# Optimization experiments

Measured on AMD Instinct MI355X. Metric: run time of the kernel, lower is better.

Reference implementation:

```python
import jax, jax.numpy as jnp
import numpy as np

N_NODES = 50000
N_EDGES = 1600000
IN_FEATS = 256
NUM_HEADS = 4
OUT_FEATS = 32
NEG_SLOPE = 0.2


def setup_inputs() -> dict:
    key = jax.random.key(0)
    k_feat, k_src, k_dst, k_w, k_al, k_ar = jax.random.split(key, 6)
    feat = jax.random.normal(k_feat, (N_NODES, IN_FEATS), dtype=jnp.float32)
    src = jax.random.randint(k_src, (N_EDGES,), 0, N_NODES, dtype=jnp.int32)
    dst = jax.random.randint(k_dst, (N_EDGES,), 0, N_NODES, dtype=jnp.int32)
    # Glorot/xavier-like scales
    w_scale = np.sqrt(2.0 / (IN_FEATS + NUM_HEADS * OUT_FEATS)).astype(np.float32)
    a_scale = np.sqrt(2.0 / (1 + OUT_FEATS)).astype(np.float32)
    W_fc = jax.random.normal(k_w, (NUM_HEADS * OUT_FEATS, IN_FEATS), dtype=jnp.float32) * w_scale
    attn_l = jax.random.normal(k_al, (1, NUM_HEADS, OUT_FEATS), dtype=jnp.float32) * a_scale
    attn_r = jax.random.normal(k_ar, (1, NUM_HEADS, OUT_FEATS), dtype=jnp.float32) * a_scale
    bias = jnp.zeros((NUM_HEADS * OUT_FEATS,), dtype=jnp.float32)
    return {"feat": feat, "W_fc": W_fc, "attn_l": attn_l, "attn_r": attn_r,
            "bias": bias, "src": src, "dst": dst}


def reference(feat, W_fc, attn_l, attn_r, bias, src, dst):
    N = feat.shape[0]
    H, F = NUM_HEADS, OUT_FEATS
    # dense projection: [N, H, F]
    h = (feat @ W_fc.T).reshape(N, H, F)
    # per-node attention logits: [N, H]
    el = (h * attn_l).sum(axis=-1)
    er = (h * attn_r).sum(axis=-1)
    # u_add_v edge score + leaky relu: [E, H]
    e = el[src] + er[dst]
    e = jnp.where(e >= 0, e, NEG_SLOPE * e)
    # segment softmax over destination nodes
    m = jax.ops.segment_max(e, dst, num_segments=N)          # [N, H]
    m = jnp.where(jnp.isfinite(m), m, 0.0)                   # guard 0-in-degree
    e_exp = jnp.exp(e - m[dst])                              # [E, H]
    denom = jax.ops.segment_sum(e_exp, dst, num_segments=N)  # [N, H]
    denom = jnp.where(denom > 0, denom, 1.0)
    a = e_exp / denom[dst]                                   # [E, H]
    # weighted message aggregation: [N, H, F]
    msg = h[src] * a[:, :, None]                             # [E, H, F]
    out = jax.ops.segment_sum(msg, dst, num_segments=N)
    out = out + bias.reshape(1, H, F)
    return out
```

## Files before the change

kernel.cpp:

```cpp
#include <hip/hip_runtime.h>

typedef __attribute__((ext_vector_type(8))) short bf16x8;
typedef __attribute__((ext_vector_type(4))) float f32x4;

#define IN_F 256
#define HF 128
#define NHEADS 4
#define NEG 0.2f
#define GBM 128
#define GBK 64
#define LDK 72

#define RB 256
#define NBP 200
#define CHUNK 6400
#define ITPT 25
#define BCAP 10000

__device__ __forceinline__ unsigned short f2bf(float x) {
    unsigned u = __float_as_uint(x);
    unsigned r = (u + 0x7FFFu + ((u >> 16) & 1u)) >> 16;
    return (unsigned short)r;
}
__device__ __forceinline__ float bf2f(unsigned short b) {
    return __uint_as_float((unsigned)b << 16);
}

__global__ __launch_bounds__(256) void gemm_kernel(const float* __restrict__ feat,
                                                   const float* __restrict__ W,
                                                   unsigned short* __restrict__ hb, int N) {
    __shared__ unsigned short As[GBM][LDK];
    __shared__ unsigned short Bs[HF][LDK];
    const int t = threadIdx.x;
    const int n0 = blockIdx.x * GBM;
    const int lane = t & 63;
    const int wid = t >> 6;
    const int wm = (wid >> 1) * 64;
    const int wn = (wid & 1) * 64;
    const int lr = lane & 15;
    const int lk = (lane >> 4) * 8;

    f32x4 acc[4][4];
#pragma unroll
    for (int i = 0; i < 4; i++)
#pragma unroll
        for (int j = 0; j < 4; j++) acc[i][j] = (f32x4){0.f, 0.f, 0.f, 0.f};

    for (int k0 = 0; k0 < IN_F; k0 += GBK) {
#pragma unroll
        for (int r = 0; r < 4; r++) {
            int idx = t + r * 256;
            int row = idx >> 3;
            int c8 = (idx & 7) * 8;
            int n = n0 + row;
            float4 v0 = make_float4(0.f, 0.f, 0.f, 0.f), v1 = v0;
            if (n < N) {
                v0 = *(const float4*)&feat[(size_t)n * IN_F + k0 + c8];
                v1 = *(const float4*)&feat[(size_t)n * IN_F + k0 + c8 + 4];
            }
            bf16x8 sa;
            sa[0] = f2bf(v0.x); sa[1] = f2bf(v0.y); sa[2] = f2bf(v0.z); sa[3] = f2bf(v0.w);
            sa[4] = f2bf(v1.x); sa[5] = f2bf(v1.y); sa[6] = f2bf(v1.z); sa[7] = f2bf(v1.w);
            *(bf16x8*)&As[row][c8] = sa;
            float4 w0 = *(const float4*)&W[(size_t)row * IN_F + k0 + c8];
            float4 w1 = *(const float4*)&W[(size_t)row * IN_F + k0 + c8 + 4];
            bf16x8 sb;
            sb[0] = f2bf(w0.x); sb[1] = f2bf(w0.y); sb[2] = f2bf(w0.z); sb[3] = f2bf(w0.w);
            sb[4] = f2bf(w1.x); sb[5] = f2bf(w1.y); sb[6] = f2bf(w1.z); sb[7] = f2bf(w1.w);
            *(bf16x8*)&Bs[row][c8] = sb;
        }
        __syncthreads();
#pragma unroll
        for (int ks = 0; ks < 2; ks++) {
            bf16x8 a[4], b[4];
#pragma unroll
            for (int mi = 0; mi < 4; mi++) a[mi] = *(bf16x8*)&As[wm + mi * 16 + lr][ks * 32 + lk];
#pragma unroll
            for (int ni = 0; ni < 4; ni++) b[ni] = *(bf16x8*)&Bs[wn + ni * 16 + lr][ks * 32 + lk];
#pragma unroll
            for (int mi = 0; mi < 4; mi++)
#pragma unroll
                for (int ni = 0; ni < 4; ni++)
                    acc[mi][ni] = __builtin_amdgcn_mfma_f32_16x16x32_bf16(a[mi], b[ni], acc[mi][ni], 0, 0, 0);
        }
        __syncthreads();
    }
    const int crow = (lane >> 4) * 4;
#pragma unroll
    for (int mi = 0; mi < 4; mi++)
#pragma unroll
        for (int j = 0; j < 4; j++) {
            int n = n0 + wm + mi * 16 + crow + j;
            if (n < N) {
#pragma unroll
                for (int ni = 0; ni < 4; ni++) {
                    int o = wn + ni * 16 + lr;
                    hb[(size_t)n * HF + o] = f2bf(acc[mi][ni][j]);
                }
            }
        }
}

__global__ __launch_bounds__(256) void elr_kernel(const unsigned short* __restrict__ hb,
                                                  const float* __restrict__ al,
                                                  const float* __restrict__ ar,
                                                  float* __restrict__ el,
                                                  float* __restrict__ er, int N) {
    int g = blockIdx.x * 256 + threadIdx.x;
    int n = g >> 5;
    int ll = g & 31;
    if (n >= N) return;
    int o4 = ll * 4;
    ushort4 v = *(const ushort4*)&hb[(size_t)n * HF + o4];
    float4 a = *(const float4*)&al[o4];
    float4 r = *(const float4*)&ar[o4];
    float h0 = bf2f(v.x), h1 = bf2f(v.y), h2 = bf2f(v.z), h3 = bf2f(v.w);
    float l = h0 * a.x + h1 * a.y + h2 * a.z + h3 * a.w;
    float rr = h0 * r.x + h1 * r.y + h2 * r.z + h3 * r.w;
#pragma unroll
    for (int off = 4; off >= 1; off >>= 1) {
        l += __shfl_xor(l, off);
        rr += __shfl_xor(rr, off);
    }
    if ((ll & 7) == 0) {
        int head = ll >> 3;
        el[n * NHEADS + head] = l;
        er[n * NHEADS + head] = rr;
    }
}

__global__ __launch_bounds__(256) void part_kernel(const int* __restrict__ src,
                                                   const int* __restrict__ dst,
                                                   int* __restrict__ ebuf,
                                                   int* __restrict__ cntArr,
                                                   int* __restrict__ ofsArr, int E) {
    __shared__ int cnt[256];
    __shared__ int sc[256];
    __shared__ int cur[256];
    __shared__ int stage[CHUNK];
    const int blk = blockIdx.x, t = threadIdx.x;
    const int eb = blk * CHUNK;
    cnt[t] = 0;
    __syncthreads();

    int bkt[ITPT], ent[ITPT];
#pragma unroll
    for (int i = 0; i < ITPT; i++) {
        int idx = eb + i * 256 + t;
        int b = NBP - 1, e = 0;
        if (idx < E) {
            int d = dst[idx];
            int s = src[idx];
            b = d >> 8;
            e = s | ((d & 255) << 24);
        }
        bkt[i] = b;
        ent[i] = e;
        atomicAdd(&cnt[b], 1);
    }
    __syncthreads();
    int orig = cnt[t];
    sc[t] = orig;
    __syncthreads();
    for (int off = 1; off < 256; off <<= 1) {
        int v = (t >= off) ? sc[t - off] : 0;
        __syncthreads();
        sc[t] += v;
        __syncthreads();
    }
    int excl = sc[t] - orig;
    if (t < NBP) {
        cntArr[blk * NBP + t] = orig;
        ofsArr[blk * NBP + t] = excl;
    }
    cur[t] = excl;
    __syncthreads();
#pragma unroll
    for (int i = 0; i < ITPT; i++) {
        int pos = atomicAdd(&cur[bkt[i]], 1);
        stage[pos] = ent[i];
    }
    __syncthreads();
#pragma unroll
    for (int i = 0; i < ITPT; i++) {
        int idx = i * 256 + t;
        ebuf[eb + idx] = stage[idx];
    }
}

__global__ __launch_bounds__(256) void bscan_kernel(const int* __restrict__ cntArr,
                                                    int* __restrict__ bucketStart, int nblk) {
    __shared__ int sums[256];
    const int t = threadIdx.x;
    int s = 0;
    if (t < NBP)
        for (int blk = 0; blk < nblk; blk++) s += cntArr[blk * NBP + t];
    sums[t] = s;
    __syncthreads();
    for (int off = 1; off < 256; off <<= 1) {
        int v = (t >= off) ? sums[t - off] : 0;
        __syncthreads();
        sums[t] += v;
        __syncthreads();
    }
    if (t < NBP) bucketStart[t] = sums[t] - s;
}

__global__ __launch_bounds__(256) void bsort_kernel(const int* __restrict__ ebuf,
                                                    const int* __restrict__ cntArr,
                                                    const int* __restrict__ ofsArr,
                                                    const int* __restrict__ bucketStart,
                                                    int* __restrict__ rowStart,
                                                    int* __restrict__ esrc,
                                                    int nblk, int N, int E) {
    __shared__ int lcnt[256];
    __shared__ int lsc[256];
    __shared__ int lcur[256];
    __shared__ int sorted[BCAP];
    const int b = blockIdx.x, t = threadIdx.x;
    const int gbase = bucketStart[b];
    lcnt[t] = 0;
    __syncthreads();

    int rbase = 0, rlen = 0;
    if (t < nblk) {
        rbase = t * CHUNK + ofsArr[t * NBP + b];
        rlen = cntArr[t * NBP + b];
    }
    int i = 0;
    for (; i + 3 < rlen; i += 4) {
        unsigned e0 = (unsigned)ebuf[rbase + i];
        unsigned e1 = (unsigned)ebuf[rbase + i + 1];
        unsigned e2 = (unsigned)ebuf[rbase + i + 2];
        unsigned e3 = (unsigned)ebuf[rbase + i + 3];
        atomicAdd(&lcnt[e0 >> 24], 1);
        atomicAdd(&lcnt[e1 >> 24], 1);
        atomicAdd(&lcnt[e2 >> 24], 1);
        atomicAdd(&lcnt[e3 >> 24], 1);
    }
    for (; i < rlen; i++) {
        unsigned e = (unsigned)ebuf[rbase + i];
        atomicAdd(&lcnt[e >> 24], 1);
    }
    __syncthreads();
    int orig = lcnt[t];
    lsc[t] = orig;
    __syncthreads();
    for (int off = 1; off < 256; off <<= 1) {
        int v = (t >= off) ? lsc[t - off] : 0;
        __syncthreads();
        lsc[t] += v;
        __syncthreads();
    }
    int excl = lsc[t] - orig;
    int node = b * RB + t;
    if (node < N) rowStart[node] = gbase + excl;
    if (b == 0 && t == 0) rowStart[N] = E;
    lcur[t] = excl;
    __syncthreads();
    i = 0;
    for (; i + 3 < rlen; i += 4) {
        unsigned e0 = (unsigned)ebuf[rbase + i];
        unsigned e1 = (unsigned)ebuf[rbase + i + 1];
        unsigned e2 = (unsigned)ebuf[rbase + i + 2];
        unsigned e3 = (unsigned)ebuf[rbase + i + 3];
        sorted[atomicAdd(&lcur[e0 >> 24], 1)] = (int)(e0 & 0xFFFFFFu);
        sorted[atomicAdd(&lcur[e1 >> 24], 1)] = (int)(e1 & 0xFFFFFFu);
        sorted[atomicAdd(&lcur[e2 >> 24], 1)] = (int)(e2 & 0xFFFFFFu);
        sorted[atomicAdd(&lcur[e3 >> 24], 1)] = (int)(e3 & 0xFFFFFFu);
    }
    for (; i < rlen; i++) {
        unsigned e = (unsigned)ebuf[rbase + i];
        sorted[atomicAdd(&lcur[e >> 24], 1)] = (int)(e & 0xFFFFFFu);
    }
    __syncthreads();
    const int total = lsc[255];
    for (int k = t; k < total; k += 256) esrc[gbase + k] = sorted[k];
}

__global__ __launch_bounds__(256) void agg_kernel(const int* __restrict__ rowStart,
                                                  const int* __restrict__ esrc,
                                                  const unsigned short* __restrict__ hb,
                                                  const float* __restrict__ el,
                                                  const float* __restrict__ er,
                                                  const float* __restrict__ bias,
                                                  float* __restrict__ out, int N) {
    const int wid = threadIdx.x >> 6;
    const int lane = threadIdx.x & 63;
    const int n = blockIdx.x * 4 + wid;
    if (n >= N) return;
    const int lg = lane & 15;
    const int grp = lane >> 4;
    const int head = lg >> 2;
    const float ern = er[n * NHEADS + head];
    const int beg = rowStart[n];
    const int end = rowStart[n + 1];

    float acc[8];
#pragma unroll
    for (int i = 0; i < 8; i++) acc[i] = 0.f;
    float den = 0.f;

#pragma unroll 2
    for (int j = beg + grp; j < end; j += 4) {
        int s = esrc[j];
        float x = el[s * NHEADS + head] + ern;
        x = x >= 0.f ? x : NEG * x;
        float sv = __expf(x);
        uint4 hv = *(const uint4*)&hb[(size_t)s * HF + lg * 8];
        acc[0] += sv * bf2f((unsigned short)(hv.x & 0xFFFFu));
        acc[1] += sv * bf2f((unsigned short)(hv.x >> 16));
        acc[2] += sv * bf2f((unsigned short)(hv.y & 0xFFFFu));
        acc[3] += sv * bf2f((unsigned short)(hv.y >> 16));
        acc[4] += sv * bf2f((unsigned short)(hv.z & 0xFFFFu));
        acc[5] += sv * bf2f((unsigned short)(hv.z >> 16));
        acc[6] += sv * bf2f((unsigned short)(hv.w & 0xFFFFu));
        acc[7] += sv * bf2f((unsigned short)(hv.w >> 16));
        den += sv;
    }

#pragma unroll
    for (int off = 16; off < 64; off <<= 1) {
#pragma unroll
        for (int i = 0; i < 8; i++) acc[i] += __shfl_xor(acc[i], off);
        den += __shfl_xor(den, off);
    }

    if (lane < 16) {
        float inv = 1.f / (den > 0.f ? den : 1.f);
        float4 b0 = *(const float4*)&bias[lg * 8];
        float4 b1 = *(const float4*)&bias[lg * 8 + 4];
        float4 o0, o1;
        o0.x = acc[0] * inv + b0.x; o0.y = acc[1] * inv + b0.y;
        o0.z = acc[2] * inv + b0.z; o0.w = acc[3] * inv + b0.w;
        o1.x = acc[4] * inv + b1.x; o1.y = acc[5] * inv + b1.y;
        o1.z = acc[6] * inv + b1.z; o1.w = acc[7] * inv + b1.w;
        *(float4*)&out[(size_t)n * HF + lg * 8] = o0;
        *(float4*)&out[(size_t)n * HF + lg * 8 + 4] = o1;
    }
}

extern "C" void kernel_launch(void* const* d_in, const int* in_sizes, int n_in,
                              void* d_out, int out_size, void* d_ws, size_t ws_size,
                              hipStream_t stream) {
    const float* feat = (const float*)d_in[0];
    const float* W    = (const float*)d_in[1];
    const float* al   = (const float*)d_in[2];
    const float* ar   = (const float*)d_in[3];
    const float* bias = (const float*)d_in[4];
    const int*   src  = (const int*)d_in[5];
    const int*   dst  = (const int*)d_in[6];
    const int N = in_sizes[0] / IN_F;
    const int E = in_sizes[5];
    float* out = (float*)d_out;

    const int nblk = (E + CHUNK - 1) / CHUNK;
    const int NBUCK = (N + RB - 1) / RB;

    unsigned short* hb = (unsigned short*)d_ws;
    float* el       = (float*)(hb + (size_t)N * HF);
    float* er       = el + (size_t)N * NHEADS;
    int* rowStart   = (int*)(er + (size_t)N * NHEADS);
    int* esrc       = rowStart + (N + 1);
    int* ebuf       = esrc + E;
    int* cntArr     = ebuf + (size_t)nblk * CHUNK;
    int* ofsArr     = cntArr + (size_t)nblk * NBP;
    int* bucketStart= ofsArr + (size_t)nblk * NBP;

    gemm_kernel<<<(N + GBM - 1) / GBM, 256, 0, stream>>>(feat, W, hb, N);
    elr_kernel<<<((size_t)N * 32 + 255) / 256, 256, 0, stream>>>(hb, al, ar, el, er, N);
    part_kernel<<<nblk, 256, 0, stream>>>(src, dst, ebuf, cntArr, ofsArr, E);
    bscan_kernel<<<1, 256, 0, stream>>>(cntArr, bucketStart, nblk);
    bsort_kernel<<<NBUCK, 256, 0, stream>>>(ebuf, cntArr, ofsArr, bucketStart,
                                            rowStart, esrc, nblk, N, E);
    agg_kernel<<<(N + 3) / 4, 256, 0, stream>>>(rowStart, esrc, hb, el, er, bias, out, N);
}
```

Before: 143.8 us.

## Fuse attention-logit reduction into GEMM epilogue and co-launch edge partitioning

The separate el/er kernel is removed. The per-head attention logits are now computed from the fp32 MFMA accumulators in the GEMM epilogue, using cross-lane shuffles and a shared-memory staging buffer, which avoids re-reading the bf16 projection from global memory. The GEMM blocks and the edge-partition blocks now run as one launch, split by block index, so the two independent stages can overlap and a launch is saved. In exchange, dynamic shared memory is sized for the GEMM, so partition blocks reserve more LDS than before, and the logits now come from unrounded fp32 accumulators, which shifts them slightly numerically.

```diff
diff --git a/kernel.cpp b/kernel.cpp
--- a/kernel.cpp
+++ b/kernel.cpp
@@ -17,6 +17,8 @@
 #define ITPT 25
 #define BCAP 10000
 
+#define FUSED_SMEM (GBM * LDK * 2 * 2)
+
 __device__ __forceinline__ unsigned short f2bf(float x) {
     unsigned u = __float_as_uint(x);
     unsigned r = (u + 0x7FFFu + ((u >> 16) & 1u)) >> 16;
@@ -26,165 +28,181 @@
     return __uint_as_float((unsigned)b << 16);
 }
 
-__global__ __launch_bounds__(256) void gemm_kernel(const float* __restrict__ feat,
-                                                   const float* __restrict__ W,
-                                                   unsigned short* __restrict__ hb, int N) {
-    __shared__ unsigned short As[GBM][LDK];
-    __shared__ unsigned short Bs[HF][LDK];
+__global__ __launch_bounds__(256) void fused1_kernel(
+    const float* __restrict__ feat, const float* __restrict__ W,
+    const float* __restrict__ al, const float* __restrict__ ar,
+    unsigned short* __restrict__ hb, float* __restrict__ el, float* __restrict__ er,
+    const int* __restrict__ src, const int* __restrict__ dst,
+    int* __restrict__ ebuf, int* __restrict__ cntArr, int* __restrict__ ofsArr,
+    int N, int E, int GG)
+{
+    extern __shared__ char smem[];
     const int t = threadIdx.x;
-    const int n0 = blockIdx.x * GBM;
-    const int lane = t & 63;
-    const int wid = t >> 6;
-    const int wm = (wid >> 1) * 64;
-    const int wn = (wid & 1) * 64;
-    const int lr = lane & 15;
-    const int lk = (lane >> 4) * 8;
-
-    f32x4 acc[4][4];
-#pragma unroll
-    for (int i = 0; i < 4; i++)
-#pragma unroll
-        for (int j = 0; j < 4; j++) acc[i][j] = (f32x4){0.f, 0.f, 0.f, 0.f};
-
-    for (int k0 = 0; k0 < IN_F; k0 += GBK) {
-#pragma unroll
-        for (int r = 0; r < 4; r++) {
-            int idx = t + r * 256;
-            int row = idx >> 3;
-            int c8 = (idx & 7) * 8;
-            int n = n0 + row;
-            float4 v0 = make_float4(0.f, 0.f, 0.f, 0.f), v1 = v0;
+
+    if ((int)blockIdx.x < GG) {
+        unsigned short (*As)[LDK] = (unsigned short(*)[LDK])smem;
+        unsigned short (*Bs)[LDK] = (unsigned short(*)[LDK])(smem + GBM * LDK * 2);
+        const int n0 = blockIdx.x * GBM;
+        const int lane = t & 63;
+        const int wid = t >> 6;
+        const int wm = (wid >> 1) * 64;
+        const int wn = (wid & 1) * 64;
+        const int lr = lane & 15;
+        const int lk = (lane >> 4) * 8;
+
+        f32x4 acc[4][4];
+#pragma unroll
+        for (int i = 0; i < 4; i++)
+#pragma unroll
+            for (int j = 0; j < 4; j++) acc[i][j] = (f32x4){0.f, 0.f, 0.f, 0.f};
+
+        for (int k0 = 0; k0 < IN_F; k0 += GBK) {
+#pragma unroll
+            for (int r = 0; r < 4; r++) {
+                int idx = t + r * 256;
+                int row = idx >> 3;
+                int c8 = (idx & 7) * 8;
+                int n = n0 + row;
+                float4 v0 = make_float4(0.f, 0.f, 0.f, 0.f), v1 = v0;
+                if (n < N) {
+                    v0 = *(const float4*)&feat[(size_t)n * IN_F + k0 + c8];
+                    v1 = *(const float4*)&feat[(size_t)n * IN_F + k0 + c8 + 4];
+                }
+                bf16x8 sa;
+                sa[0] = f2bf(v0.x); sa[1] = f2bf(v0.y); sa[2] = f2bf(v0.z); sa[3] = f2bf(v0.w);
+                sa[4] = f2bf(v1.x); sa[5] = f2bf(v1.y); sa[6] = f2bf(v1.z); sa[7] = f2bf(v1.w);
+                *(bf16x8*)&As[row][c8] = sa;
+                float4 w0 = *(const float4*)&W[(size_t)row * IN_F + k0 + c8];
+                float4 w1 = *(const float4*)&W[(size_t)row * IN_F + k0 + c8 + 4];
+                bf16x8 sb;
+                sb[0] = f2bf(w0.x); sb[1] = f2bf(w0.y); sb[2] = f2bf(w0.z); sb[3] = f2bf(w0.w);
+                sb[4] = f2bf(w1.x); sb[5] = f2bf(w1.y); sb[6] = f2bf(w1.z); sb[7] = f2bf(w1.w);
+                *(bf16x8*)&Bs[row][c8] = sb;
+            }
+            __syncthreads();
+#pragma unroll
+            for (int ks = 0; ks < 2; ks++) {
+                bf16x8 a[4], b[4];
+#pragma unroll
+                for (int mi = 0; mi < 4; mi++) a[mi] = *(bf16x8*)&As[wm + mi * 16 + lr][ks * 32 + lk];
+#pragma unroll
+                for (int ni = 0; ni < 4; ni++) b[ni] = *(bf16x8*)&Bs[wn + ni * 16 + lr][ks * 32 + lk];
+#pragma unroll
+                for (int mi = 0; mi < 4; mi++)
+#pragma unroll
+                    for (int ni = 0; ni < 4; ni++)
+                        acc[mi][ni] = __builtin_amdgcn_mfma_f32_16x16x32_bf16(a[mi], b[ni], acc[mi][ni], 0, 0, 0);
+            }
+            __syncthreads();
+        }
+        const int crow = (lane >> 4) * 4;
+#pragma unroll
+        for (int mi = 0; mi < 4; mi++)
+#pragma unroll
+            for (int j = 0; j < 4; j++) {
+                int n = n0 + wm + mi * 16 + crow + j;
+                if (n < N) {
+#pragma unroll
+                    for (int ni = 0; ni < 4; ni++) {
+                        int o = wn + ni * 16 + lr;
+                        hb[(size_t)n * HF + o] = f2bf(acc[mi][ni][j]);
+                    }
+                }
+            }
+        float al_c[4], ar_c[4];
+#pragma unroll
+        for (int ni = 0; ni < 4; ni++) {
+            int o = wn + ni * 16 + lr;
+            al_c[ni] = al[o];
+            ar_c[ni] = ar[o];
+        }
+        float* elp = (float*)smem;
+        float* erp = elp + 128 * 4;
+        const int h0 = wn >> 5;
+#pragma unroll
+        for (int mi = 0; mi < 4; mi++)
+#pragma unroll
+            for (int j = 0; j < 4; j++) {
+                float e0 = acc[mi][0][j] * al_c[0] + acc[mi][1][j] * al_c[1];
+                float e1 = acc[mi][2][j] * al_c[2] + acc[mi][3][j] * al_c[3];
+                float r0 = acc[mi][0][j] * ar_c[0] + acc[mi][1][j] * ar_c[1];
+                float r1 = acc[mi][2][j] * ar_c[2] + acc[mi][3][j] * ar_c[3];
+#pragma unroll
+                for (int off = 1; off < 16; off <<= 1) {
+                    e0 += __shfl_xor(e0, off);
+                    e1 += __shfl_xor(e1, off);
+                    r0 += __shfl_xor(r0, off);
+                    r1 += __shfl_xor(r1, off);
+                }
+                if (lr == 0) {
+                    int row = wm + mi * 16 + crow + j;
+                    elp[row * 4 + h0]     = e0;
+                    elp[row * 4 + h0 + 1] = e1;
+                    erp[row * 4 + h0]     = r0;
+                    erp[row * 4 + h0 + 1] = r1;
+                }
+            }
+        __syncthreads();
+        if (t < 128) {
+            int n = n0 + t;
             if (n < N) {
-                v0 = *(const float4*)&feat[(size_t)n * IN_F + k0 + c8];
-                v1 = *(const float4*)&feat[(size_t)n * IN_F + k0 + c8 + 4];
-            }
-            bf16x8 sa;
-            sa[0] = f2bf(v0.x); sa[1] = f2bf(v0.y); sa[2] = f2bf(v0.z); sa[3] = f2bf(v0.w);
-            sa[4] = f2bf(v1.x); sa[5] = f2bf(v1.y); sa[6] = f2bf(v1.z); sa[7] = f2bf(v1.w);
-            *(bf16x8*)&As[row][c8] = sa;
-            float4 w0 = *(const float4*)&W[(size_t)row * IN_F + k0 + c8];
-            float4 w1 = *(const float4*)&W[(size_t)row * IN_F + k0 + c8 + 4];
-            bf16x8 sb;
-            sb[0] = f2bf(w0.x); sb[1] = f2bf(w0.y); sb[2] = f2bf(w0.z); sb[3] = f2bf(w0.w);
-            sb[4] = f2bf(w1.x); sb[5] = f2bf(w1.y); sb[6] = f2bf(w1.z); sb[7] = f2bf(w1.w);
-            *(bf16x8*)&Bs[row][c8] = sb;
-        }
-        __syncthreads();
-#pragma unroll
-        for (int ks = 0; ks < 2; ks++) {
-            bf16x8 a[4], b[4];
-#pragma unroll
-            for (int mi = 0; mi < 4; mi++) a[mi] = *(bf16x8*)&As[wm + mi * 16 + lr][ks * 32 + lk];
-#pragma unroll
-            for (int ni = 0; ni < 4; ni++) b[ni] = *(bf16x8*)&Bs[wn + ni * 16 + lr][ks * 32 + lk];
-#pragma unroll
-            for (int mi = 0; mi < 4; mi++)
-#pragma unroll
-                for (int ni = 0; ni < 4; ni++)
-                    acc[mi][ni] = __builtin_amdgcn_mfma_f32_16x16x32_bf16(a[mi], b[ni], acc[mi][ni], 0, 0, 0);
-        }
-        __syncthreads();
-    }
-    const int crow = (lane >> 4) * 4;
-#pragma unroll
-    for (int mi = 0; mi < 4; mi++)
-#pragma unroll
-        for (int j = 0; j < 4; j++) {
-            int n = n0 + wm + mi * 16 + crow + j;
-            if (n < N) {
-#pragma unroll
-                for (int ni = 0; ni < 4; ni++) {
-                    int o = wn + ni * 16 + lr;
-                    hb[(size_t)n * HF + o] = f2bf(acc[mi][ni][j]);
-                }
-            }
-        }
-}
-
-__global__ __launch_bounds__(256) void elr_kernel(const unsigned short* __restrict__ hb,
-                                                  const float* __restrict__ al,
-                                                  const float* __restrict__ ar,
-                                                  float* __restrict__ el,
-                                                  float* __restrict__ er, int N) {
-    int g = blockIdx.x * 256 + threadIdx.x;
-    int n = g >> 5;
-    int ll = g & 31;
-    if (n >= N) return;
-    int o4 = ll * 4;
-    ushort4 v = *(const ushort4*)&hb[(size_t)n * HF + o4];
-    float4 a = *(const float4*)&al[o4];
-    float4 r = *(const float4*)&ar[o4];
-    float h0 = bf2f(v.x), h1 = bf2f(v.y), h2 = bf2f(v.z), h3 = bf2f(v.w);
-    float l = h0 * a.x + h1 * a.y + h2 * a.z + h3 * a.w;
-    float rr = h0 * r.x + h1 * r.y + h2 * r.z + h3 * r.w;
-#pragma unroll
-    for (int off = 4; off >= 1; off >>= 1) {
-        l += __shfl_xor(l, off);
-        rr += __shfl_xor(rr, off);
-    }
-    if ((ll & 7) == 0) {
-        int head = ll >> 3;
-        el[n * NHEADS + head] = l;
-        er[n * NHEADS + head] = rr;
-    }
-}
-
-__global__ __launch_bounds__(256) void part_kernel(const int* __restrict__ src,
-                                                   const int* __restrict__ dst,
-                                                   int* __restrict__ ebuf,
-                                                   int* __restrict__ cntArr,
-                                                   int* __restrict__ ofsArr, int E) {
-    __shared__ int cnt[256];
-    __shared__ int sc[256];
-    __shared__ int cur[256];
-    __shared__ int stage[CHUNK];
-    const int blk = blockIdx.x, t = threadIdx.x;
-    const int eb = blk * CHUNK;
-    cnt[t] = 0;
-    __syncthreads();
-
-    int bkt[ITPT], ent[ITPT];
-#pragma unroll
-    for (int i = 0; i < ITPT; i++) {
-        int idx = eb + i * 256 + t;
-        int b = NBP - 1, e = 0;
-        if (idx < E) {
-            int d = dst[idx];
-            int s = src[idx];
-            b = d >> 8;
-            e = s | ((d & 255) << 24);
-        }
-        bkt[i] = b;
-        ent[i] = e;
-        atomicAdd(&cnt[b], 1);
-    }
-    __syncthreads();
-    int orig = cnt[t];
-    sc[t] = orig;
-    __syncthreads();
-    for (int off = 1; off < 256; off <<= 1) {
-        int v = (t >= off) ? sc[t - off] : 0;
-        __syncthreads();
-        sc[t] += v;
-        __syncthreads();
-    }
-    int excl = sc[t] - orig;
-    if (t < NBP) {
-        cntArr[blk * NBP + t] = orig;
-        ofsArr[blk * NBP + t] = excl;
-    }
-    cur[t] = excl;
-    __syncthreads();
-#pragma unroll
-    for (int i = 0; i < ITPT; i++) {
-        int pos = atomicAdd(&cur[bkt[i]], 1);
-        stage[pos] = ent[i];
-    }
-    __syncthreads();
-#pragma unroll
-    for (int i = 0; i < ITPT; i++) {
-        int idx = i * 256 + t;
-        ebuf[eb + idx] = stage[idx];
+                *(float4*)&el[(size_t)n * 4] = *(float4*)&elp[t * 4];
+                *(float4*)&er[(size_t)n * 4] = *(float4*)&erp[t * 4];
+            }
+        }
+    } else {
+        int* cnt = (int*)smem;
+        int* sc  = cnt + 256;
+        int* cur = sc + 256;
+        int* stage = cur + 256;
+        const int blk = blockIdx.x - GG;
+        const int eb = blk * CHUNK;
+        cnt[t] = 0;
+        __syncthreads();
+
+        int bkt[ITPT], ent[ITPT];
+#pragma unroll
+        for (int i = 0; i < ITPT; i++) {
+            int idx = eb + i * 256 + t;
+            int b = NBP - 1, e = 0;
+            if (idx < E) {
+                int d = dst[idx];
+                int s = src[idx];
+                b = d >> 8;
+                e = s | ((d & 255) << 24);
+            }
+            bkt[i] = b;
+            ent[i] = e;
+            atomicAdd(&cnt[b], 1);
+        }
+        __syncthreads();
+        int orig = cnt[t];
+        sc[t] = orig;
+        __syncthreads();
+        for (int off = 1; off < 256; off <<= 1) {
+            int v = (t >= off) ? sc[t - off] : 0;
+            __syncthreads();
+            sc[t] += v;
+            __syncthreads();
+        }
+        int excl = sc[t] - orig;
+        if (t < NBP) {
+            cntArr[blk * NBP + t] = orig;
+            ofsArr[blk * NBP + t] = excl;
+        }
+        cur[t] = excl;
+        __syncthreads();
+#pragma unroll
+        for (int i = 0; i < ITPT; i++) {
+            int pos = atomicAdd(&cur[bkt[i]], 1);
+            stage[pos] = ent[i];
+        }
+        __syncthreads();
+#pragma unroll
+        for (int i = 0; i < ITPT; i++) {
+            int idx = i * 256 + t;
+            ebuf[eb + idx] = stage[idx];
+        }
     }
 }
 
@@ -356,6 +374,7 @@
 
     const int nblk = (E + CHUNK - 1) / CHUNK;
     const int NBUCK = (N + RB - 1) / RB;
+    const int GG = (N + GBM - 1) / GBM;
 
     unsigned short* hb = (unsigned short*)d_ws;
     float* el       = (float*)(hb + (size_t)N * HF);
@@ -367,9 +386,8 @@
     int* ofsArr     = cntArr + (size_t)nblk * NBP;
     int* bucketStart= ofsArr + (size_t)nblk * NBP;
 
-    gemm_kernel<<<(N + GBM - 1) / GBM, 256, 0, stream>>>(feat, W, hb, N);
-    elr_kernel<<<((size_t)N * 32 + 255) / 256, 256, 0, stream>>>(hb, al, ar, el, er, N);
-    part_kernel<<<nblk, 256, 0, stream>>>(src, dst, ebuf, cntArr, ofsArr, E);
+    fused1_kernel<<<GG + nblk, 256, FUSED_SMEM, stream>>>(
+        feat, W, al, ar, hb, el, er, src, dst, ebuf, cntArr, ofsArr, N, E, GG);
     bscan_kernel<<<1, 256, 0, stream>>>(cntArr, bucketStart, nblk);
     bsort_kernel<<<NBUCK, 256, 0, stream>>>(ebuf, cntArr, ofsArr, bucketStart,
                                             rowStart, esrc, nblk, N, E);
```

Result: faster. 140.9 us (-2.0%).
